# Optimization experiments

Hardware: AMD Instinct MI355X
Metric: run time of the kernel (lower is better)

The kernel has to match this reference:

```python
import jax, jax.numpy as jnp
import numpy as np

N = 1024
H = 128
W = 128
SH_DEG = 3
K = (SH_DEG + 1) ** 2  # 16

C0 = 0.28209479177387814
C1 = 0.4886025119029199
C2 = (1.0925484305920792, -1.0925484305920792, 0.31539156525252005, -1.0925484305920792, 0.5462742152960396)
C3 = (-0.5900435899266435, 2.890611442640554, -0.4570457994644658, 0.3731763325901154, -0.4570457994644658, 1.445305721320277, -0.5900435899266435)


def setup_inputs() -> dict:
    key = jax.random.key(0)
    ks = jax.random.split(key, 8)
    xy = jax.random.uniform(ks[0], (N, 2), minval=-2.0, maxval=2.0)
    z = jax.random.uniform(ks[1], (N, 1), minval=2.0, maxval=8.0)
    means3D = jnp.concatenate([xy, z], axis=1)
    sh = jax.random.normal(ks[2], (N, K, 3)) * 0.3
    opacities = jax.random.uniform(ks[3], (N,), minval=0.1, maxval=1.0)
    scales = jax.random.uniform(ks[4], (N, 3), minval=0.02, maxval=0.15)
    rotations = jax.random.normal(ks[5], (N, 4))
    cam_pos = jnp.zeros((3,), jnp.float32)
    cam_rot = jnp.eye(3, dtype=jnp.float32)  # world-to-camera rotation
    tan_half_fov = jnp.array([0.7], jnp.float32)
    bg_color = jax.random.uniform(ks[6], (3,))
    near_far = jnp.array([0.2, 100.0], jnp.float32)
    return dict(means3D=means3D, sh=sh, opacities=opacities, scales=scales,
                rotations=rotations, cam_pos=cam_pos, cam_rot=cam_rot,
                tan_half_fov=tan_half_fov, bg_color=bg_color, near_far=near_far,
                image_h=H, image_w=W, sh_degree=SH_DEG)


def _eval_sh(sh, dirs):
    # degree-3 real spherical harmonics, as in the 3DGS CUDA rasterizer
    x, y, z = dirs[:, 0:1], dirs[:, 1:2], dirs[:, 2:3]
    res = C0 * sh[:, 0]
    res = res - C1 * y * sh[:, 1] + C1 * z * sh[:, 2] - C1 * x * sh[:, 3]
    xx, yy, zz = x * x, y * y, z * z
    xy, yz, xz = x * y, y * z, x * z
    res = (res + C2[0] * xy * sh[:, 4] + C2[1] * yz * sh[:, 5]
           + C2[2] * (2.0 * zz - xx - yy) * sh[:, 6]
           + C2[3] * xz * sh[:, 7] + C2[4] * (xx - yy) * sh[:, 8])
    res = (res + C3[0] * y * (3.0 * xx - yy) * sh[:, 9]
           + C3[1] * xy * z * sh[:, 10]
           + C3[2] * y * (4.0 * zz - xx - yy) * sh[:, 11]
           + C3[3] * z * (2.0 * zz - 3.0 * xx - 3.0 * yy) * sh[:, 12]
           + C3[4] * x * (4.0 * zz - xx - yy) * sh[:, 13]
           + C3[5] * z * (xx - yy) * sh[:, 14]
           + C3[6] * x * (xx - 3.0 * yy) * sh[:, 15])
    return jnp.maximum(res + 0.5, 0.0)


def _quat_to_rot(q):
    q = q / jnp.linalg.norm(q, axis=1, keepdims=True)
    r, x, y, z = q[:, 0], q[:, 1], q[:, 2], q[:, 3]
    R = jnp.stack([
        1 - 2 * (y * y + z * z), 2 * (x * y - r * z), 2 * (x * z + r * y),
        2 * (x * y + r * z), 1 - 2 * (x * x + z * z), 2 * (y * z - r * x),
        2 * (x * z - r * y), 2 * (y * z + r * x), 1 - 2 * (x * x + y * y)],
        axis=1).reshape(-1, 3, 3)
    return R


def _forward(means3D, sh, opacities, scales, rotations, cam_pos, cam_rot,
             tan_half_fov, bg_color, near_far, image_h, image_w):
    thf = tan_half_fov[0]
    fx = image_w / (2.0 * thf)
    fy = image_h / (2.0 * thf)
    # view-space positions
    t = jnp.einsum('ij,nj->ni', cam_rot, means3D - cam_pos)  # [N,3]
    tz = t[:, 2]
    lim = 1.3 * thf
    tx = jnp.clip(t[:, 0] / tz, -lim, lim) * tz
    ty = jnp.clip(t[:, 1] / tz, -lim, lim) * tz
    # 3D covariance from quaternion + scale: Sigma = (R S)(R S)^T
    Rq = _quat_to_rot(rotations)
    M = Rq * scales[:, None, :]
    cov3 = jnp.einsum('nij,nkj->nik', M, M)
    # EWA splatting: 2D covariance via projection Jacobian
    z2 = tz * tz
    zeros = jnp.zeros_like(tz)
    J = jnp.stack([
        jnp.stack([fx / tz, zeros, -fx * tx / z2], axis=1),
        jnp.stack([zeros, fy / tz, -fy * ty / z2], axis=1)], axis=1)  # [N,2,3]
    T = jnp.einsum('nij,jk->nik', J, cam_rot)
    cov2 = jnp.einsum('nij,njk,nlk->nil', T, cov3, T)  # [N,2,2]
    a = cov2[:, 0, 0] + 0.3  # low-pass filter on diagonal (as in 3DGS)
    c = cov2[:, 1, 1] + 0.3
    b = cov2[:, 0, 1]
    det = a * c - b * b
    inv_det = 1.0 / det
    conA, conB, conC = c * inv_det, -b * inv_det, a * inv_det
    # 2D means in pixel coordinates
    mx = fx * t[:, 0] / tz + (image_w - 1.0) / 2.0
    my = fy * t[:, 1] / tz + (image_h - 1.0) / 2.0
    # view-dependent color from SH
    dirs = means3D - cam_pos
    dirs = dirs / jnp.linalg.norm(dirs, axis=1, keepdims=True)
    colors = _eval_sh(sh, dirs)  # [N,3]
    # per-pixel gaussian alpha [N, P]
    pxs = jnp.arange(image_w, dtype=jnp.float32)
    pys = jnp.arange(image_h, dtype=jnp.float32)
    gy, gx = jnp.meshgrid(pys, pxs, indexing='ij')
    px = gx.reshape(-1)
    py = gy.reshape(-1)
    dx = px[None, :] - mx[:, None]
    dy = py[None, :] - my[:, None]
    power = -0.5 * (conA[:, None] * dx * dx + conC[:, None] * dy * dy) - conB[:, None] * dx * dy
    alpha = jnp.minimum(opacities[:, None] * jnp.exp(power), 0.99)
    valid = (tz > near_far[0]) & (tz < near_far[1]) & (det > 0.0)
    alpha = jnp.where(valid[:, None] & (power <= 0.0) & (alpha >= 1.0 / 255.0), alpha, 0.0)
    # global depth sort + front-to-back alpha compositing
    order = jnp.argsort(tz)
    alpha_s = alpha[order]
    colors_s = colors[order]
    trans = jnp.cumprod(1.0 - alpha_s, axis=0)  # inclusive transmittance [N,P]
    trans_excl = jnp.concatenate([jnp.ones((1, alpha_s.shape[1]), alpha_s.dtype), trans[:-1]], axis=0)
    wgt = alpha_s * trans_excl  # blending weights
    img = jnp.einsum('np,nc->pc', wgt, colors_s) + trans[-1][:, None] * bg_color[None, :]
    return img.reshape(image_h, image_w, 3).transpose(2, 0, 1)  # [3,H,W]


def reference(means3D, sh, opacities, scales, rotations, cam_pos, cam_rot,
              tan_half_fov, bg_color, near_far, image_h, image_w, sh_degree):
    # sh_degree is fixed to 3 via the SH table size (K=16); kept for signature parity
    return _forward(means3D, sh, opacities, scales, rotations, cam_pos, cam_rot,
                    tan_half_fov, bg_color, near_far, image_h, image_w)
```

## Files before the change

### kernel.cpp

```cpp
#include <hip/hip_runtime.h>

#define NG   1024
#define IMH  128
#define IMW  128
#define NPIX (IMH * IMW)
#define SEGS 16

__global__ __launch_bounds__(256) void k_prep(
    const float* __restrict__ means,
    const float* __restrict__ sh,
    const float* __restrict__ opac,
    const float* __restrict__ scales,
    const float* __restrict__ rots,
    const float* __restrict__ campos,
    const float* __restrict__ camrot,
    const float* __restrict__ thf_p,
    const float* __restrict__ nearfar,
    float4* __restrict__ g0, float4* __restrict__ g1, float4* __restrict__ g2)
{
    __shared__ unsigned long long lk[NG];
    __shared__ int prank[4 * 64];

    int t = threadIdx.x;
    int b = blockIdx.x;

    float thf = thf_p[0];
    float R[9];
    #pragma unroll
    for (int k = 0; k < 9; k++) R[k] = camrot[k];
    float cp0 = campos[0], cp1 = campos[1], cp2 = campos[2];
    float near_ = nearfar[0], far_ = nearfar[1];

    #pragma unroll
    for (int j = 0; j < 4; j++) {
        int g = j * 256 + t;
        float dx = means[3 * g + 0] - cp0;
        float dy = means[3 * g + 1] - cp1;
        float dz = means[3 * g + 2] - cp2;
        float tzk = R[6] * dx + R[7] * dy + R[8] * dz;
        unsigned u = __float_as_uint(tzk);
        u = (u & 0x80000000u) ? ~u : (u | 0x80000000u);
        lk[g] = ((unsigned long long)u << 32) | (unsigned)g;
    }
    __syncthreads();

    int li    = t & 63;
    int chunk = t >> 6;
    int gi    = b * 64 + li;
    unsigned long long ki = lk[gi];
    int cnt = 0;
    int j0 = chunk * 256;
    #pragma unroll 8
    for (int j = 0; j < 256; j++) cnt += (lk[j0 + j] < ki) ? 1 : 0;
    prank[chunk * 64 + li] = cnt;
    __syncthreads();

    if (t < 64) {
        int i = b * 64 + t;
        float fx = IMW / (2.0f * thf);
        float fy = IMH / (2.0f * thf);

        float d0x = means[3 * i + 0] - cp0;
        float d0y = means[3 * i + 1] - cp1;
        float d0z = means[3 * i + 2] - cp2;

        float tx0 = R[0] * d0x + R[1] * d0y + R[2] * d0z;
        float ty0 = R[3] * d0x + R[4] * d0y + R[5] * d0z;
        float tz  = R[6] * d0x + R[7] * d0y + R[8] * d0z;

        float lim  = 1.3f * thf;
        float invz = 1.0f / tz;
        float txc  = fminf(fmaxf(tx0 * invz, -lim), lim) * tz;
        float tyc  = fminf(fmaxf(ty0 * invz, -lim), lim) * tz;

        float qr = rots[4 * i + 0], qx = rots[4 * i + 1];
        float qy = rots[4 * i + 2], qz = rots[4 * i + 3];
        float qn = rsqrtf(qr * qr + qx * qx + qy * qy + qz * qz);
        qr *= qn; qx *= qn; qy *= qn; qz *= qn;
        float Rq0 = 1.0f - 2.0f * (qy * qy + qz * qz);
        float Rq1 = 2.0f * (qx * qy - qr * qz);
        float Rq2 = 2.0f * (qx * qz + qr * qy);
        float Rq3 = 2.0f * (qx * qy + qr * qz);
        float Rq4 = 1.0f - 2.0f * (qx * qx + qz * qz);
        float Rq5 = 2.0f * (qy * qz - qr * qx);
        float Rq6 = 2.0f * (qx * qz - qr * qy);
        float Rq7 = 2.0f * (qy * qz + qr * qx);
        float Rq8 = 1.0f - 2.0f * (qx * qx + qy * qy);

        float sx = scales[3 * i + 0], sy = scales[3 * i + 1], sz = scales[3 * i + 2];
        float M0 = Rq0 * sx, M1 = Rq1 * sy, M2 = Rq2 * sz;
        float M3 = Rq3 * sx, M4 = Rq4 * sy, M5 = Rq5 * sz;
        float M6 = Rq6 * sx, M7 = Rq7 * sy, M8 = Rq8 * sz;

        float c00 = M0 * M0 + M1 * M1 + M2 * M2;
        float c01 = M0 * M3 + M1 * M4 + M2 * M5;
        float c02 = M0 * M6 + M1 * M7 + M2 * M8;
        float c11 = M3 * M3 + M4 * M4 + M5 * M5;
        float c12 = M3 * M6 + M4 * M7 + M5 * M8;
        float c22 = M6 * M6 + M7 * M7 + M8 * M8;

        float z2  = tz * tz;
        float J00 = fx * invz, J02 = -fx * txc / z2;
        float J11 = fy * invz, J12 = -fy * tyc / z2;

        float T00 = J00 * R[0] + J02 * R[6];
        float T01 = J00 * R[1] + J02 * R[7];
        float T02 = J00 * R[2] + J02 * R[8];
        float T10 = J11 * R[3] + J12 * R[6];
        float T11 = J11 * R[4] + J12 * R[7];
        float T12 = J11 * R[5] + J12 * R[8];

        float v00 = T00 * c00 + T01 * c01 + T02 * c02;
        float v01 = T00 * c01 + T01 * c11 + T02 * c12;
        float v02 = T00 * c02 + T01 * c12 + T02 * c22;
        float v10 = T10 * c00 + T11 * c01 + T12 * c02;
        float v11 = T10 * c01 + T11 * c11 + T12 * c12;
        float v12 = T10 * c02 + T11 * c12 + T12 * c22;

        float a = v00 * T00 + v01 * T01 + v02 * T02 + 0.3f;
        float bb = v00 * T10 + v01 * T11 + v02 * T12;
        float c = v10 * T10 + v11 * T11 + v12 * T12 + 0.3f;

        float det    = a * c - bb * bb;
        float invdet = 1.0f / det;
        float conA = c * invdet, conB = -bb * invdet, conC = a * invdet;

        float mx = fx * tx0 * invz + (IMW - 1) * 0.5f;
        float my = fy * ty0 * invz + (IMH - 1) * 0.5f;

        float dn = rsqrtf(d0x * d0x + d0y * d0y + d0z * d0z);
        float x = d0x * dn, y = d0y * dn, z = d0z * dn;
        float xx = x * x, yy = y * y, zz = z * z;
        float xy = x * y, yz = y * z, xz = x * z;

        float basis[16];
        basis[0]  = 0.28209479177387814f;
        basis[1]  = -0.4886025119029199f * y;
        basis[2]  =  0.4886025119029199f * z;
        basis[3]  = -0.4886025119029199f * x;
        basis[4]  =  1.0925484305920792f * xy;
        basis[5]  = -1.0925484305920792f * yz;
        basis[6]  =  0.31539156525252005f * (2.0f * zz - xx - yy);
        basis[7]  = -1.0925484305920792f * xz;
        basis[8]  =  0.5462742152960396f * (xx - yy);
        basis[9]  = -0.5900435899266435f * y * (3.0f * xx - yy);
        basis[10] =  2.890611442640554f * xy * z;
        basis[11] = -0.4570457994644658f * y * (4.0f * zz - xx - yy);
        basis[12] =  0.3731763325901154f * z * (2.0f * zz - 3.0f * xx - 3.0f * yy);
        basis[13] = -0.4570457994644658f * x * (4.0f * zz - xx - yy);
        basis[14] =  1.445305721320277f * z * (xx - yy);
        basis[15] = -0.5900435899266435f * x * (xx - 3.0f * yy);

        const float* shp = sh + i * 48;
        float col[3];
        #pragma unroll
        for (int ch = 0; ch < 3; ch++) {
            float res = 0.0f;
            #pragma unroll
            for (int k = 0; k < 16; k++) res += basis[k] * shp[k * 3 + ch];
            col[ch] = fmaxf(res + 0.5f, 0.0f);
        }

        bool valid = (tz > near_) && (tz < far_) && (det > 0.0f);
        float op = valid ? opac[i] : 0.0f;

        float rx, ry;
        if (op >= (1.0f / 255.0f)) {
            float s2 = 2.0f * logf(255.0f * op);
            rx = sqrtf(s2 * a) + 1e-3f;
            ry = sqrtf(s2 * c) + 1e-3f;
        } else {
            rx = -1.0f; ry = -1.0f;
        }

        int r = prank[0 * 64 + t] + prank[1 * 64 + t] +
                prank[2 * 64 + t] + prank[3 * 64 + t];

        g0[r] = make_float4(mx, my, rx, ry);
        g1[r] = make_float4(-0.5f * conA, -conB, -0.5f * conC, op);
        g2[r] = make_float4(col[0], col[1], col[2], 0.0f);
    }
}

__global__ __launch_bounds__(1024) void k_comp(
    const float4* __restrict__ g0, const float4* __restrict__ g1,
    const float4* __restrict__ g2, const float* __restrict__ bg,
    float* __restrict__ out)
{
    __shared__ float4 lA[NG];
    __shared__ float4 lB[NG];
    __shared__ float  lC[NG];
    __shared__ float4 red[SEGS * 64];
    __shared__ int wcnt[16];

    int t    = threadIdx.x;
    int wid  = t >> 6;
    int lane = t & 63;
    int bx = blockIdx.x & 15, by = blockIdx.x >> 4;
    float x0 = (float)(bx * 8), y0 = (float)(by * 8);

    float4 c0 = g0[t];
    bool surv = (c0.z >= 0.0f) &&
                (c0.x + c0.z >= x0) && (c0.x - c0.z <= x0 + 7.0f) &&
                (c0.y + c0.w >= y0) && (c0.y - c0.w <= y0 + 7.0f);
    unsigned long long m = __ballot(surv);
    if (lane == 0) wcnt[wid] = __popcll(m);
    __syncthreads();

    int pre = 0, M = 0;
    #pragma unroll
    for (int w = 0; w < 16; w++) {
        int cw = wcnt[w];
        M += cw;
        if (w < wid) pre += cw;
    }
    if (surv) {
        int pos = pre + __popcll(m & ((1ull << lane) - 1ull));
        float4 c1 = g1[t];
        float4 c2 = g2[t];
        lA[pos] = make_float4(c0.x, c0.y, c1.x, c1.y);
        lB[pos] = make_float4(c1.z, c1.w, c2.x, c2.y);
        lC[pos] = c2.z;
    }
    __syncthreads();

    M = __builtin_amdgcn_readfirstlane(M);
    int len = (M + SEGS - 1) / SEGS;
    int seg = __builtin_amdgcn_readfirstlane(wid);
    int ks  = seg * len;
    int ke  = min(M, ks + len);

    float fpx = x0 + (float)(lane & 7);
    float fpy = y0 + (float)(lane >> 3);

    float T = 1.0f, cr = 0.0f, cg = 0.0f, cb = 0.0f;
    for (int k = ks; k < ke; k++) {
        float4 qA = lA[k];
        float4 qB = lB[k];
        float  qc = lC[k];
        float dx = fpx - qA.x;
        float dy = fpy - qA.y;
        float pw = fmaf(dx, fmaf(qA.z, dx, qA.w * dy), qB.x * (dy * dy));
        float al = qB.y * __expf(pw);
        al = fminf(al, 0.99f);
        bool ok = (pw <= 0.0f) && (al >= (1.0f / 255.0f));
        al = ok ? al : 0.0f;
        float w = al * T;
        cr = fmaf(w, qB.z, cr);
        cg = fmaf(w, qB.w, cg);
        cb = fmaf(w, qc, cb);
        T = fmaf(-al, T, T);
    }

    red[seg * 64 + lane] = make_float4(cr, cg, cb, T);
    __syncthreads();

    if (t < 64) {
        float Tt = 1.0f, r = 0.0f, g = 0.0f, b = 0.0f;
        #pragma unroll
        for (int s = 0; s < SEGS; s++) {
            float4 v = red[s * 64 + t];
            r = fmaf(Tt, v.x, r);
            g = fmaf(Tt, v.y, g);
            b = fmaf(Tt, v.z, b);
            Tt *= v.w;
        }
        int pix = (by * 8 + (t >> 3)) * IMW + bx * 8 + (t & 7);
        out[0 * NPIX + pix] = r + Tt * bg[0];
        out[1 * NPIX + pix] = g + Tt * bg[1];
        out[2 * NPIX + pix] = b + Tt * bg[2];
    }
}

extern "C" void kernel_launch(void* const* d_in, const int* in_sizes, int n_in,
                              void* d_out, int out_size, void* d_ws, size_t ws_size,
                              hipStream_t stream)
{
    (void)in_sizes; (void)n_in; (void)out_size; (void)ws_size;

    const float* means   = (const float*)d_in[0];
    const float* sh      = (const float*)d_in[1];
    const float* opac    = (const float*)d_in[2];
    const float* scales  = (const float*)d_in[3];
    const float* rots    = (const float*)d_in[4];
    const float* campos  = (const float*)d_in[5];
    const float* camrot  = (const float*)d_in[6];
    const float* thf     = (const float*)d_in[7];
    const float* bg      = (const float*)d_in[8];
    const float* nearfar = (const float*)d_in[9];

    char* ws = (char*)d_ws;
    float4* g0 = (float4*)(ws + 0);
    float4* g1 = (float4*)(ws + 16384);
    float4* g2 = (float4*)(ws + 32768);

    k_prep<<<16, 256, 0, stream>>>(means, sh, opac, scales, rots, campos,
                                   camrot, thf, nearfar, g0, g1, g2);
    k_comp<<<256, 1024, 0, stream>>>(g0, g1, g2, bg, (float*)d_out);
}
```

Measured before the change: 87.20 us.

## Composite each 8x8 tile with a single wavefront instead of sixteen segments

The compositing kernel moves from 1024-thread blocks that split the culled Gaussian list into 16 depth segments and merge them through shared memory to 64-thread blocks. In the new version one wavefront culls all 1024 Gaussians in a loop and composites the whole list serially. This removes the block-wide barriers, the cross-wave reduction and most of the intra-block parallelism. The serial loop per pixel becomes up to 16x longer, and only 256 wavefronts cover the GPU, so latency hiding and occupancy drop sharply.

```diff
diff --git a/kernel.cpp b/kernel.cpp
--- a/kernel.cpp
+++ b/kernel.cpp
@@ -4,7 +4,6 @@
 #define IMH  128
 #define IMW  128
 #define NPIX (IMH * IMW)
-#define SEGS 16
 
 __global__ __launch_bounds__(256) void k_prep(
     const float* __restrict__ means,
@@ -182,7 +181,7 @@
     }
 }
 
-__global__ __launch_bounds__(1024) void k_comp(
+__global__ __launch_bounds__(64) void k_comp(
     const float4* __restrict__ g0, const float4* __restrict__ g1,
     const float4* __restrict__ g2, const float* __restrict__ bg,
     float* __restrict__ out)
@@ -190,51 +189,38 @@
     __shared__ float4 lA[NG];
     __shared__ float4 lB[NG];
     __shared__ float  lC[NG];
-    __shared__ float4 red[SEGS * 64];
-    __shared__ int wcnt[16];
-
-    int t    = threadIdx.x;
-    int wid  = t >> 6;
-    int lane = t & 63;
+
+    int lane = threadIdx.x;
     int bx = blockIdx.x & 15, by = blockIdx.x >> 4;
     float x0 = (float)(bx * 8), y0 = (float)(by * 8);
 
-    float4 c0 = g0[t];
-    bool surv = (c0.z >= 0.0f) &&
-                (c0.x + c0.z >= x0) && (c0.x - c0.z <= x0 + 7.0f) &&
-                (c0.y + c0.w >= y0) && (c0.y - c0.w <= y0 + 7.0f);
-    unsigned long long m = __ballot(surv);
-    if (lane == 0) wcnt[wid] = __popcll(m);
-    __syncthreads();
-
-    int pre = 0, M = 0;
-    #pragma unroll
-    for (int w = 0; w < 16; w++) {
-        int cw = wcnt[w];
-        M += cw;
-        if (w < wid) pre += cw;
-    }
-    if (surv) {
-        int pos = pre + __popcll(m & ((1ull << lane) - 1ull));
-        float4 c1 = g1[t];
-        float4 c2 = g2[t];
-        lA[pos] = make_float4(c0.x, c0.y, c1.x, c1.y);
-        lB[pos] = make_float4(c1.z, c1.w, c2.x, c2.y);
-        lC[pos] = c2.z;
-    }
-    __syncthreads();
-
-    M = __builtin_amdgcn_readfirstlane(M);
-    int len = (M + SEGS - 1) / SEGS;
-    int seg = __builtin_amdgcn_readfirstlane(wid);
-    int ks  = seg * len;
-    int ke  = min(M, ks + len);
+    int base = 0;
+    #pragma unroll 4
+    for (int r = 0; r < 16; r++) {
+        int gidx = r * 64 + lane;
+        float4 c0 = g0[gidx];
+        bool surv = (c0.z >= 0.0f) &&
+                    (c0.x + c0.z >= x0) && (c0.x - c0.z <= x0 + 7.0f) &&
+                    (c0.y + c0.w >= y0) && (c0.y - c0.w <= y0 + 7.0f);
+        unsigned long long m = __ballot(surv);
+        if (surv) {
+            int pos = base + __popcll(m & ((1ull << lane) - 1ull));
+            float4 c1 = g1[gidx];
+            float4 c2 = g2[gidx];
+            lA[pos] = make_float4(c0.x, c0.y, c1.x, c1.y);
+            lB[pos] = make_float4(c1.z, c1.w, c2.x, c2.y);
+            lC[pos] = c2.z;
+        }
+        base += __popcll(m);
+    }
+    int M = base;
 
     float fpx = x0 + (float)(lane & 7);
     float fpy = y0 + (float)(lane >> 3);
-
     float T = 1.0f, cr = 0.0f, cg = 0.0f, cb = 0.0f;
-    for (int k = ks; k < ke; k++) {
+
+    #pragma unroll 2
+    for (int k = 0; k < M; k++) {
         float4 qA = lA[k];
         float4 qB = lB[k];
         float  qc = lC[k];
@@ -252,24 +238,10 @@
         T = fmaf(-al, T, T);
     }
 
-    red[seg * 64 + lane] = make_float4(cr, cg, cb, T);
-    __syncthreads();
-
-    if (t < 64) {
-        float Tt = 1.0f, r = 0.0f, g = 0.0f, b = 0.0f;
-        #pragma unroll
-        for (int s = 0; s < SEGS; s++) {
-            float4 v = red[s * 64 + t];
-            r = fmaf(Tt, v.x, r);
-            g = fmaf(Tt, v.y, g);
-            b = fmaf(Tt, v.z, b);
-            Tt *= v.w;
-        }
-        int pix = (by * 8 + (t >> 3)) * IMW + bx * 8 + (t & 7);
-        out[0 * NPIX + pix] = r + Tt * bg[0];
-        out[1 * NPIX + pix] = g + Tt * bg[1];
-        out[2 * NPIX + pix] = b + Tt * bg[2];
-    }
+    int pix = (by * 8 + (lane >> 3)) * IMW + bx * 8 + (lane & 7);
+    out[0 * NPIX + pix] = cr + T * bg[0];
+    out[1 * NPIX + pix] = cg + T * bg[1];
+    out[2 * NPIX + pix] = cb + T * bg[2];
 }
 
 extern "C" void kernel_launch(void* const* d_in, const int* in_sizes, int n_in,
@@ -296,5 +268,5 @@
 
     k_prep<<<16, 256, 0, stream>>>(means, sh, opac, scales, rots, campos,
                                    camrot, thf, nearfar, g0, g1, g2);
-    k_comp<<<256, 1024, 0, stream>>>(g0, g1, g2, bg, (float*)d_out);
+    k_comp<<<256, 64, 0, stream>>>(g0, g1, g2, bg, (float*)d_out);
 }
```

After: 96.12 us. 10.2% more time.

## Spread prep over more blocks, vectorize SH loads, hoist compositing loads

Applied to the files above, without the earlier changes.

The preprocessing kernel now runs 64 blocks of 256 threads, each handling 16 Gaussians, instead of 16 blocks handling 64. Each thread's rank-counting slice shrinks to 64 keys, which shortens the serial projection phase per block and spreads it over more CUs. SH coefficients and quaternions are now read as float4 vectors, and the colour dot product is fused into one loop over three accumulators. In the compositing kernel the g1/g2 loads are issued unconditionally, before the ballot, so they overlap with the culling test. The cost is some redundant global reads of rejected Gaussians and more blocks each redoing the 1024-key shared-memory fill.

```diff
diff --git a/kernel.cpp b/kernel.cpp
--- a/kernel.cpp
+++ b/kernel.cpp
@@ -19,7 +19,7 @@
     float4* __restrict__ g0, float4* __restrict__ g1, float4* __restrict__ g2)
 {
     __shared__ unsigned long long lk[NG];
-    __shared__ int prank[4 * 64];
+    __shared__ int prank[16][16];
 
     int t = threadIdx.x;
     int b = blockIdx.x;
@@ -44,21 +44,24 @@
     }
     __syncthreads();
 
-    int li    = t & 63;
-    int chunk = t >> 6;
-    int gi    = b * 64 + li;
-    unsigned long long ki = lk[gi];
+    int gl    = t & 15;
+    int chunk = t >> 4;
+    unsigned long long ki = lk[b * 16 + gl];
     int cnt = 0;
-    int j0 = chunk * 256;
+    int j0 = chunk * 64;
     #pragma unroll 8
-    for (int j = 0; j < 256; j++) cnt += (lk[j0 + j] < ki) ? 1 : 0;
-    prank[chunk * 64 + li] = cnt;
-    __syncthreads();
-
-    if (t < 64) {
-        int i = b * 64 + t;
+    for (int j = 0; j < 64; j++) cnt += (lk[j0 + j] < ki) ? 1 : 0;
+    prank[chunk][gl] = cnt;
+    __syncthreads();
+
+    if (t < 16) {
+        int i = b * 16 + t;
         float fx = IMW / (2.0f * thf);
         float fy = IMH / (2.0f * thf);
+
+        int r = 0;
+        #pragma unroll
+        for (int c2i = 0; c2i < 16; c2i++) r += prank[c2i][t];
 
         float d0x = means[3 * i + 0] - cp0;
         float d0y = means[3 * i + 1] - cp1;
@@ -73,8 +76,8 @@
         float txc  = fminf(fmaxf(tx0 * invz, -lim), lim) * tz;
         float tyc  = fminf(fmaxf(ty0 * invz, -lim), lim) * tz;
 
-        float qr = rots[4 * i + 0], qx = rots[4 * i + 1];
-        float qy = rots[4 * i + 2], qz = rots[4 * i + 3];
+        float4 q = ((const float4*)rots)[i];
+        float qr = q.x, qx = q.y, qy = q.z, qz = q.w;
         float qn = rsqrtf(qr * qr + qx * qx + qy * qy + qz * qz);
         qr *= qn; qx *= qn; qy *= qn; qz *= qn;
         float Rq0 = 1.0f - 2.0f * (qy * qy + qz * qz);
@@ -117,9 +120,9 @@
         float v11 = T10 * c01 + T11 * c11 + T12 * c12;
         float v12 = T10 * c02 + T11 * c12 + T12 * c22;
 
-        float a = v00 * T00 + v01 * T01 + v02 * T02 + 0.3f;
+        float a  = v00 * T00 + v01 * T01 + v02 * T02 + 0.3f;
         float bb = v00 * T10 + v01 * T11 + v02 * T12;
-        float c = v10 * T10 + v11 * T11 + v12 * T12 + 0.3f;
+        float c  = v10 * T10 + v11 * T11 + v12 * T12 + 0.3f;
 
         float det    = a * c - bb * bb;
         float invdet = 1.0f / det;
@@ -151,15 +154,24 @@
         basis[14] =  1.445305721320277f * z * (xx - yy);
         basis[15] = -0.5900435899266435f * x * (xx - 3.0f * yy);
 
-        const float* shp = sh + i * 48;
-        float col[3];
+        float f[48];
+        {
+            const float4* sh4 = (const float4*)(sh + i * 48);
+            float4* fv = (float4*)f;
+            #pragma unroll
+            for (int j = 0; j < 12; j++) fv[j] = sh4[j];
+        }
+        float colr = 0.0f, colg = 0.0f, colb = 0.0f;
         #pragma unroll
-        for (int ch = 0; ch < 3; ch++) {
-            float res = 0.0f;
-            #pragma unroll
-            for (int k = 0; k < 16; k++) res += basis[k] * shp[k * 3 + ch];
-            col[ch] = fmaxf(res + 0.5f, 0.0f);
+        for (int k = 0; k < 16; k++) {
+            float bk = basis[k];
+            colr = fmaf(bk, f[3 * k + 0], colr);
+            colg = fmaf(bk, f[3 * k + 1], colg);
+            colb = fmaf(bk, f[3 * k + 2], colb);
         }
+        colr = fmaxf(colr + 0.5f, 0.0f);
+        colg = fmaxf(colg + 0.5f, 0.0f);
+        colb = fmaxf(colb + 0.5f, 0.0f);
 
         bool valid = (tz > near_) && (tz < far_) && (det > 0.0f);
         float op = valid ? opac[i] : 0.0f;
@@ -173,12 +185,9 @@
             rx = -1.0f; ry = -1.0f;
         }
 
-        int r = prank[0 * 64 + t] + prank[1 * 64 + t] +
-                prank[2 * 64 + t] + prank[3 * 64 + t];
-
         g0[r] = make_float4(mx, my, rx, ry);
         g1[r] = make_float4(-0.5f * conA, -conB, -0.5f * conC, op);
-        g2[r] = make_float4(col[0], col[1], col[2], 0.0f);
+        g2[r] = make_float4(colr, colg, colb, 0.0f);
     }
 }
 
@@ -200,6 +209,8 @@
     float x0 = (float)(bx * 8), y0 = (float)(by * 8);
 
     float4 c0 = g0[t];
+    float4 c1 = g1[t];
+    float4 c2 = g2[t];
     bool surv = (c0.z >= 0.0f) &&
                 (c0.x + c0.z >= x0) && (c0.x - c0.z <= x0 + 7.0f) &&
                 (c0.y + c0.w >= y0) && (c0.y - c0.w <= y0 + 7.0f);
@@ -216,8 +227,6 @@
     }
     if (surv) {
         int pos = pre + __popcll(m & ((1ull << lane) - 1ull));
-        float4 c1 = g1[t];
-        float4 c2 = g2[t];
         lA[pos] = make_float4(c0.x, c0.y, c1.x, c1.y);
         lB[pos] = make_float4(c1.z, c1.w, c2.x, c2.y);
         lC[pos] = c2.z;
@@ -294,7 +303,7 @@
     float4* g1 = (float4*)(ws + 16384);
     float4* g2 = (float4*)(ws + 32768);
 
-    k_prep<<<16, 256, 0, stream>>>(means, sh, opac, scales, rots, campos,
+    k_prep<<<64, 256, 0, stream>>>(means, sh, opac, scales, rots, campos,
                                    camrot, thf, nearfar, g0, g1, g2);
     k_comp<<<256, 1024, 0, stream>>>(g0, g1, g2, bg, (float*)d_out);
 }
```

New measurement: 85.53 us. About the same (-1.9%).
